# Kernel tuning notes

Hardware: AMD Instinct MI355X
Metric: run time of the kernel (lower is better)

## Reference

```python
import jax, jax.numpy as jnp
import numpy as np

VOCAB, EMBED, HIDDEN = 32000, 1024, 1024
BATCH, SEQ = 64, 128
PAD_IDX = 0


def setup_inputs() -> dict:
    key = jax.random.key(0)
    k_in, k_emb, k_wih, k_whh, k_bih, k_bhh = jax.random.split(key, 6)
    inputs = jax.random.randint(k_in, (BATCH, SEQ), 0, VOCAB)
    emb = jax.random.normal(k_emb, (VOCAB, EMBED), dtype=jnp.float32)
    emb = emb.at[PAD_IDX].set(0.0)  # nn.Embedding zeros the padding_idx row
    s = 1.0 / np.sqrt(HIDDEN).astype(np.float32)  # torch LSTMCell init bound
    W_ih = jax.random.uniform(k_wih, (4 * HIDDEN, EMBED), minval=-s, maxval=s, dtype=jnp.float32)
    W_hh = jax.random.uniform(k_whh, (4 * HIDDEN, HIDDEN), minval=-s, maxval=s, dtype=jnp.float32)
    b_ih = jax.random.uniform(k_bih, (4 * HIDDEN,), minval=-s, maxval=s, dtype=jnp.float32)
    b_hh = jax.random.uniform(k_bhh, (4 * HIDDEN,), minval=-s, maxval=s, dtype=jnp.float32)
    return {"emb": emb, "W_ih": W_ih, "W_hh": W_hh, "b_ih": b_ih, "b_hh": b_hh, "inputs": inputs}


def reference(emb, W_ih, W_hh, b_ih, b_hh, inputs):
    # Embedding lookup: [B, S, E] -> time-major [S, B, E]
    x = jnp.swapaxes(emb[inputs], 0, 1)
    B = inputs.shape[0]
    H = W_hh.shape[1]
    h0 = jnp.zeros((B, H), dtype=emb.dtype)
    c0 = jnp.zeros((B, H), dtype=emb.dtype)

    def step(carry, xt):
        h, c = carry
        # torch LSTMCell gate order: i, f, g, o
        gates = xt @ W_ih.T + b_ih + h @ W_hh.T + b_hh  # [B, 4H]
        i, f, g, o = jnp.split(gates, 4, axis=-1)
        i = jax.nn.sigmoid(i)
        f = jax.nn.sigmoid(f)
        g = jnp.tanh(g)
        o = jax.nn.sigmoid(o)
        c2 = f * c + i * g
        h2 = o * jnp.tanh(c2)
        # NOTE: original's h_c_mask is all-zeros (its fill loop only writes
        # zeros), so torch.where always selects the new state -> no masking.
        return (h2, c2), None

    (h, c), _ = jax.lax.scan(step, (h0, c0), x)
    return (h, c)
```

## Files before the change

### kernel.cpp

```cpp
#include <hip/hip_runtime.h>
#include <hip/hip_bf16.h>

#define EMB   1024
#define HID   1024
#define NBATCH 64
#define SEQ   128
#define NGATE 4096
#define NBLK  128

typedef __attribute__((ext_vector_type(8))) short bf16x8;
typedef __attribute__((ext_vector_type(4))) float f32x4;

__device__ __forceinline__ unsigned short f2bf(float f) {
    unsigned int u = __float_as_uint(f);
    unsigned int r = (u + 0x7FFFu + ((u >> 16) & 1u)) >> 16;
    return (unsigned short)r;
}

__device__ __forceinline__ bf16x8 pack8(float4 a, float4 b) {
    bf16x8 r;
    r[0] = (short)f2bf(a.x); r[1] = (short)f2bf(a.y);
    r[2] = (short)f2bf(a.z); r[3] = (short)f2bf(a.w);
    r[4] = (short)f2bf(b.x); r[5] = (short)f2bf(b.y);
    r[6] = (short)f2bf(b.z); r[7] = (short)f2bf(b.w);
    return r;
}

__device__ __forceinline__ float sigmoidf_(float x) { return 1.0f / (1.0f + __expf(-x)); }
__device__ __forceinline__ float tanhf_(float x)    { return 1.0f - 2.0f / (1.0f + __expf(2.0f * x)); }


__global__ void gather_x(const float* __restrict__ emb, const int* __restrict__ inp,
                         unsigned short* __restrict__ xbf) {
    int m = blockIdx.x;
    int t = m >> 6, b = m & 63;
    int tok = inp[b * SEQ + t];
    float4 v = ((const float4*)(emb + (long)tok * EMB))[threadIdx.x];
    ushort4 o;
    o.x = f2bf(v.x); o.y = f2bf(v.y); o.z = f2bf(v.z); o.w = f2bf(v.w);
    ((ushort4*)(xbf + (long)m * EMB))[threadIdx.x] = o;
}

__global__ void conv_w(const float* __restrict__ w, unsigned short* __restrict__ wbf) {
    long i = (long)blockIdx.x * 1024 + (long)threadIdx.x * 4;
    float4 v = *(const float4*)(w + i);
    ushort4 o;
    o.x = f2bf(v.x); o.y = f2bf(v.y); o.z = f2bf(v.z); o.w = f2bf(v.w);
    *(ushort4*)(wbf + i) = o;
}

__global__ void bsum_k(const float* __restrict__ bi, const float* __restrict__ bh,
                       float* __restrict__ bs) {
    int i = blockIdx.x * 256 + threadIdx.x;
    bs[i] = bi[i] + bh[i];
}

__global__ __launch_bounds__(256) void gemm_xw(const unsigned short* __restrict__ A,
                                               const unsigned short* __restrict__ Bw,
                                               const float* __restrict__ bsum,
                                               float* __restrict__ XW) {
    __shared__ unsigned short As[128][40];
    __shared__ unsigned short Bs[128][40];
    int bx = blockIdx.x;
    int by = blockIdx.y;
    int tid = threadIdx.x;
    int w = tid >> 6, l = tid & 63;
    int wm = w >> 1, wn = w & 1;
    int lr = l & 15, lk = l >> 4;

    f32x4 acc[4][4];
#pragma unroll
    for (int ni = 0; ni < 4; ++ni) {
        float bsv = bsum[bx * 128 + wn * 64 + ni * 16 + lr];
#pragma unroll
        for (int mi = 0; mi < 4; ++mi) {
            acc[mi][ni][0] = bsv; acc[mi][ni][1] = bsv;
            acc[mi][ni][2] = bsv; acc[mi][ni][3] = bsv;
        }
    }

    int sr = tid >> 1;
    int sc = (tid & 1) * 16;
    const unsigned short* ga = A  + (long)(by * 128 + sr) * 1024 + sc;
    const unsigned short* gb = Bw + (long)(bx * 128 + sr) * 1024 + sc;

    for (int kt = 0; kt < 32; ++kt) {
        uint4 va0 = *(const uint4*)(ga);
        uint4 va1 = *(const uint4*)(ga + 8);
        uint4 vb0 = *(const uint4*)(gb);
        uint4 vb1 = *(const uint4*)(gb + 8);
        *(uint4*)&As[sr][sc]     = va0;
        *(uint4*)&As[sr][sc + 8] = va1;
        *(uint4*)&Bs[sr][sc]     = vb0;
        *(uint4*)&Bs[sr][sc + 8] = vb1;
        __syncthreads();

        bf16x8 af[4], bfr[4];
#pragma unroll
        for (int mi = 0; mi < 4; ++mi)
            af[mi] = *(const bf16x8*)&As[wm * 64 + mi * 16 + lr][lk * 8];
#pragma unroll
        for (int ni = 0; ni < 4; ++ni)
            bfr[ni] = *(const bf16x8*)&Bs[wn * 64 + ni * 16 + lr][lk * 8];
#pragma unroll
        for (int mi = 0; mi < 4; ++mi)
#pragma unroll
            for (int ni = 0; ni < 4; ++ni)
                acc[mi][ni] = __builtin_amdgcn_mfma_f32_16x16x32_bf16(af[mi], bfr[ni], acc[mi][ni], 0, 0, 0);
        __syncthreads();
        ga += 32; gb += 32;
    }

#pragma unroll
    for (int mi = 0; mi < 4; ++mi) {
        int mg = by * 128 + wm * 64 + mi * 16 + lk * 4;
        int tt = mg >> 6;
        int bb = mg & 63;
#pragma unroll
        for (int ni = 0; ni < 4; ++ni) {
            int nn = bx * 128 + wn * 64 + ni * 16 + lr;
            *(f32x4*)(XW + (long)tt * (NGATE * 64) + (long)nn * 64 + bb) = acc[mi][ni];
        }
    }
}

__global__ __launch_bounds__(512) void lstm_rec(const float* __restrict__ Whh,
                                                const float* __restrict__ XW,
                                                unsigned short* __restrict__ hseq,
                                                unsigned* __restrict__ flags,
                                                float* __restrict__ out) {
    __shared__ float Glds[32][68];
    __shared__ unsigned short Hs[64][8];

    int tid = threadIdx.x;
    int w = tid >> 6, l = tid & 63;
    int lr = l & 15, lk = l >> 4;
    int bg = w & 3, ng = w >> 2;
    int g = blockIdx.x;
    unsigned* flags1 = flags;
    unsigned* flags2 = flags + 128;
    int grp = g >> 3;
    int rep = g & 15;
    bool leader = (g & 7) == 0;

    int nl = ng * 16 + lr;
    int q = nl >> 3, u = nl & 7;
    long nrow = (long)(q * 1024 + g * 8 + u) * 1024;
    bf16x8 wf[32];
#pragma unroll
    for (int kk = 0; kk < 32; ++kk) {
        int k0 = kk * 32 + lk * 8;
        float4 w0 = *(const float4*)(Whh + nrow + k0);
        float4 w1 = *(const float4*)(Whh + nrow + k0 + 4);
        wf[kk] = pack8(w0, w1);
    }

    float c = 0.0f;
    int brow = bg * 16 + lr;

    for (int t = 0; t < SEQ; ++t) {
        const uint4* hc = (const uint4*)hseq + (long)t * 8192;

        float px[4];
#pragma unroll
        for (int qq = 0; qq < 4; ++qq)
            px[qq] = XW[(long)t * (NGATE * 64) +
                        (long)(qq * 1024 + g * 8 + w) * 64 + l];

        f32x4 acc0 = {0.f, 0.f, 0.f, 0.f}, acc1 = {0.f, 0.f, 0.f, 0.f};
#pragma unroll
        for (int kk = 0; kk < 32; kk += 2) {
            union { uint4 u4; bf16x8 v; } ua, ub;
            ua.u4 = hc[(kk * 4 + lk) * 64 + brow];
            ub.u4 = hc[((kk + 1) * 4 + lk) * 64 + brow];
            acc0 = __builtin_amdgcn_mfma_f32_16x16x32_bf16(ua.v, wf[kk],     acc0, 0, 0, 0);
            acc1 = __builtin_amdgcn_mfma_f32_16x16x32_bf16(ub.v, wf[kk + 1], acc1, 0, 0, 0);
        }
        f32x4 gacc = acc0 + acc1;
        *(f32x4*)&Glds[ng * 16 + lr][bg * 16 + lk * 4] = gacc;
        __syncthreads();

        float p[4];
#pragma unroll
        for (int qq = 0; qq < 4; ++qq)
            p[qq] = Glds[qq * 8 + w][l] + px[qq];
        float ig = sigmoidf_(p[0]);
        float fg = sigmoidf_(p[1]);
        float gg = tanhf_(p[2]);
        float og = sigmoidf_(p[3]);
        c = fg * c + ig * gg;
        float h = og * tanhf_(c);

        if (t == SEQ - 1) {
            out[l * HID + g * 8 + w] = h;
            out[NBATCH * HID + l * HID + g * 8 + w] = c;
        } else {
            Hs[l][w] = f2bf(h);
            __syncthreads();
            unsigned tv = (unsigned)(t + 1);

            if (tid < 64) {
                unsigned long long* hn = (unsigned long long*)hseq +
                                         (long)(t + 1) * 16384 + (long)g * 128;
                const unsigned long long* hsu = (const unsigned long long*)Hs;
                __hip_atomic_store(&hn[tid * 2],     hsu[tid * 2],
                                   __ATOMIC_RELAXED, __HIP_MEMORY_SCOPE_AGENT);
                __hip_atomic_store(&hn[tid * 2 + 1], hsu[tid * 2 + 1],
                                   __ATOMIC_RELAXED, __HIP_MEMORY_SCOPE_AGENT);
                asm volatile("s_waitcnt vmcnt(0)" ::: "memory");
                if (tid == 0)
                    __hip_atomic_store(&flags1[g], tv,
                                       __ATOMIC_RELAXED, __HIP_MEMORY_SCOPE_AGENT);

                if (leader) {
                    if (tid < 2) {
                        const unsigned* fp = flags1 + g + tid * 4;
                        long spins = 0;
                        for (;;) {
                            uint4 fv;
                            asm volatile("global_load_dwordx4 %0, %1, off sc0 sc1\n\t"
                                         "s_waitcnt vmcnt(0)"
                                         : "=v"(fv) : "v"(fp) : "memory");
                            __builtin_amdgcn_sched_barrier(0);
                            unsigned mn  = fv.x < fv.y ? fv.x : fv.y;
                            unsigned mn2 = fv.z < fv.w ? fv.z : fv.w;
                            if (mn2 < mn) mn = mn2;
                            if (mn >= tv) break;
                            if (++spins > 500000L) break;
                            __builtin_amdgcn_s_sleep(1);
                        }
                    }
                    if (tid < 16)
                        __hip_atomic_store(&flags2[tid * 16 + grp], tv,
                                           __ATOMIC_RELAXED, __HIP_MEMORY_SCOPE_AGENT);
                }

                if (tid < 4) {
                    const unsigned* fp = flags2 + rep * 16 + tid * 4;
                    long spins = 0;
                    for (;;) {
                        uint4 fv;
                        asm volatile("global_load_dwordx4 %0, %1, off sc0 sc1\n\t"
                                     "s_waitcnt vmcnt(0)"
                                     : "=v"(fv) : "v"(fp) : "memory");
                        __builtin_amdgcn_sched_barrier(0);
                        unsigned mn  = fv.x < fv.y ? fv.x : fv.y;
                        unsigned mn2 = fv.z < fv.w ? fv.z : fv.w;
                        if (mn2 < mn) mn = mn2;
                        if (mn >= tv) break;
                        if (++spins > 500000L) break;
                        __builtin_amdgcn_s_sleep(1);
                    }
                }
            }
            __syncthreads();
        }
    }
}

extern "C" void kernel_launch(void* const* d_in, const int* in_sizes, int n_in,
                              void* d_out, int out_size, void* d_ws, size_t ws_size,
                              hipStream_t stream) {
    const float* emb  = (const float*)d_in[0];
    const float* W_ih = (const float*)d_in[1];
    const float* W_hh = (const float*)d_in[2];
    const float* b_ih = (const float*)d_in[3];
    const float* b_hh = (const float*)d_in[4];
    const int*   inp  = (const int*)d_in[5];
    float* out = (float*)d_out;

    char* ws = (char*)d_ws;
    float*          XW   = (float*)ws;
    unsigned short* Xbf  = (unsigned short*)(ws + 134217728);
    unsigned short* Wbf  = (unsigned short*)(ws + 150994944);
    float*          bs   = (float*)(ws + 159383552);
    unsigned short* hseq = (unsigned short*)(ws + 159399936);
    unsigned*       flags= (unsigned*)(ws + 176177152);

    hipMemsetAsync(flags, 0, 1536, stream);
    hipMemsetAsync(hseq, 0, NBATCH * HID * sizeof(unsigned short), stream);
    gather_x<<<SEQ * NBATCH, 256, 0, stream>>>(emb, inp, Xbf);
    conv_w<<<NGATE, 256, 0, stream>>>(W_ih, Wbf);
    bsum_k<<<16, 256, 0, stream>>>(b_ih, b_hh, bs);
    gemm_xw<<<dim3(32, 64), 256, 0, stream>>>(Xbf, Wbf, bs, XW);
    lstm_rec<<<NBLK, 512, 0, stream>>>(W_hh, XW, hseq, flags, out);
}
```

Before: 813.3 us.

## Fuse input projection into recurrent kernel and overlap it with grid barrier wait

Removes the separate input-projection GEMM and its large fp32 intermediate, and computes each block's x·W_ih contribution inside the recurrent kernel. The contribution for step t+1 is computed with MFMA while waiting on the cross-block barrier, so it hides in what was idle spin time. Bias is now added from registers. The cost is that W_ih rows and X are reread from global memory each step instead of being held in registers, which may lengthen the critical path if the barrier wait is short.

```diff
diff --git a/kernel.cpp b/kernel.cpp
--- a/kernel.cpp
+++ b/kernel.cpp
@@ -55,77 +55,25 @@
     bs[i] = bi[i] + bh[i];
 }
 
-__global__ __launch_bounds__(256) void gemm_xw(const unsigned short* __restrict__ A,
-                                               const unsigned short* __restrict__ Bw,
-                                               const float* __restrict__ bsum,
-                                               float* __restrict__ XW) {
-    __shared__ unsigned short As[128][40];
-    __shared__ unsigned short Bs[128][40];
-    int bx = blockIdx.x;
-    int by = blockIdx.y;
-    int tid = threadIdx.x;
-    int w = tid >> 6, l = tid & 63;
-    int wm = w >> 1, wn = w & 1;
-    int lr = l & 15, lk = l >> 4;
-
-    f32x4 acc[4][4];
-#pragma unroll
-    for (int ni = 0; ni < 4; ++ni) {
-        float bsv = bsum[bx * 128 + wn * 64 + ni * 16 + lr];
-#pragma unroll
-        for (int mi = 0; mi < 4; ++mi) {
-            acc[mi][ni][0] = bsv; acc[mi][ni][1] = bsv;
-            acc[mi][ni][2] = bsv; acc[mi][ni][3] = bsv;
-        }
+__device__ __forceinline__ void accum_x(const unsigned short* __restrict__ xr,
+                                        const unsigned short* __restrict__ wr,
+                                        int lk, f32x4& a0, f32x4& a1) {
+#pragma unroll
+    for (int kk = 0; kk < 32; kk += 2) {
+        union { uint4 u4; bf16x8 v; } xa, xb, wa, wb;
+        xa.u4 = *(const uint4*)(xr + kk * 32 + lk * 8);
+        xb.u4 = *(const uint4*)(xr + (kk + 1) * 32 + lk * 8);
+        wa.u4 = *(const uint4*)(wr + kk * 32 + lk * 8);
+        wb.u4 = *(const uint4*)(wr + (kk + 1) * 32 + lk * 8);
+        a0 = __builtin_amdgcn_mfma_f32_16x16x32_bf16(xa.v, wa.v, a0, 0, 0, 0);
+        a1 = __builtin_amdgcn_mfma_f32_16x16x32_bf16(xb.v, wb.v, a1, 0, 0, 0);
     }
-
-    int sr = tid >> 1;
-    int sc = (tid & 1) * 16;
-    const unsigned short* ga = A  + (long)(by * 128 + sr) * 1024 + sc;
-    const unsigned short* gb = Bw + (long)(bx * 128 + sr) * 1024 + sc;
-
-    for (int kt = 0; kt < 32; ++kt) {
-        uint4 va0 = *(const uint4*)(ga);
-        uint4 va1 = *(const uint4*)(ga + 8);
-        uint4 vb0 = *(const uint4*)(gb);
-        uint4 vb1 = *(const uint4*)(gb + 8);
-        *(uint4*)&As[sr][sc]     = va0;
-        *(uint4*)&As[sr][sc + 8] = va1;
-        *(uint4*)&Bs[sr][sc]     = vb0;
-        *(uint4*)&Bs[sr][sc + 8] = vb1;
-        __syncthreads();
-
-        bf16x8 af[4], bfr[4];
-#pragma unroll
-        for (int mi = 0; mi < 4; ++mi)
-            af[mi] = *(const bf16x8*)&As[wm * 64 + mi * 16 + lr][lk * 8];
-#pragma unroll
-        for (int ni = 0; ni < 4; ++ni)
-            bfr[ni] = *(const bf16x8*)&Bs[wn * 64 + ni * 16 + lr][lk * 8];
-#pragma unroll
-        for (int mi = 0; mi < 4; ++mi)
-#pragma unroll
-            for (int ni = 0; ni < 4; ++ni)
-                acc[mi][ni] = __builtin_amdgcn_mfma_f32_16x16x32_bf16(af[mi], bfr[ni], acc[mi][ni], 0, 0, 0);
-        __syncthreads();
-        ga += 32; gb += 32;
-    }
-
-#pragma unroll
-    for (int mi = 0; mi < 4; ++mi) {
-        int mg = by * 128 + wm * 64 + mi * 16 + lk * 4;
-        int tt = mg >> 6;
-        int bb = mg & 63;
-#pragma unroll
-        for (int ni = 0; ni < 4; ++ni) {
-            int nn = bx * 128 + wn * 64 + ni * 16 + lr;
-            *(f32x4*)(XW + (long)tt * (NGATE * 64) + (long)nn * 64 + bb) = acc[mi][ni];
-        }
-    }
 }
 
 __global__ __launch_bounds__(512) void lstm_rec(const float* __restrict__ Whh,
-                                                const float* __restrict__ XW,
+                                                const unsigned short* __restrict__ Xbf,
+                                                const unsigned short* __restrict__ Wih,
+                                                const float* __restrict__ bsum,
                                                 unsigned short* __restrict__ hseq,
                                                 unsigned* __restrict__ flags,
                                                 float* __restrict__ out) {
@@ -154,36 +102,39 @@
         float4 w1 = *(const float4*)(Whh + nrow + k0 + 4);
         wf[kk] = pack8(w0, w1);
     }
+    const unsigned short* wr = Wih + nrow;
+
+    float bsv[4];
+#pragma unroll
+    for (int qq = 0; qq < 4; ++qq)
+        bsv[qq] = bsum[qq * 1024 + g * 8 + w];
 
     float c = 0.0f;
     int brow = bg * 16 + lr;
 
+    f32x4 axc0 = {0.f, 0.f, 0.f, 0.f}, axc1 = {0.f, 0.f, 0.f, 0.f};
+    accum_x(Xbf + (long)brow * 1024, wr, lk, axc0, axc1);
+
     for (int t = 0; t < SEQ; ++t) {
         const uint4* hc = (const uint4*)hseq + (long)t * 8192;
 
-        float px[4];
-#pragma unroll
-        for (int qq = 0; qq < 4; ++qq)
-            px[qq] = XW[(long)t * (NGATE * 64) +
-                        (long)(qq * 1024 + g * 8 + w) * 64 + l];
-
-        f32x4 acc0 = {0.f, 0.f, 0.f, 0.f}, acc1 = {0.f, 0.f, 0.f, 0.f};
+        f32x4 ah0 = {0.f, 0.f, 0.f, 0.f}, ah1 = {0.f, 0.f, 0.f, 0.f};
 #pragma unroll
         for (int kk = 0; kk < 32; kk += 2) {
             union { uint4 u4; bf16x8 v; } ua, ub;
             ua.u4 = hc[(kk * 4 + lk) * 64 + brow];
             ub.u4 = hc[((kk + 1) * 4 + lk) * 64 + brow];
-            acc0 = __builtin_amdgcn_mfma_f32_16x16x32_bf16(ua.v, wf[kk],     acc0, 0, 0, 0);
-            acc1 = __builtin_amdgcn_mfma_f32_16x16x32_bf16(ub.v, wf[kk + 1], acc1, 0, 0, 0);
+            ah0 = __builtin_amdgcn_mfma_f32_16x16x32_bf16(ua.v, wf[kk],     ah0, 0, 0, 0);
+            ah1 = __builtin_amdgcn_mfma_f32_16x16x32_bf16(ub.v, wf[kk + 1], ah1, 0, 0, 0);
         }
-        f32x4 gacc = acc0 + acc1;
+        f32x4 gacc = (axc0 + axc1) + (ah0 + ah1);
         *(f32x4*)&Glds[ng * 16 + lr][bg * 16 + lk * 4] = gacc;
         __syncthreads();
 
         float p[4];
 #pragma unroll
         for (int qq = 0; qq < 4; ++qq)
-            p[qq] = Glds[qq * 8 + w][l] + px[qq];
+            p[qq] = Glds[qq * 8 + w][l] + bsv[qq];
         float ig = sigmoidf_(p[0]);
         float fg = sigmoidf_(p[1]);
         float gg = tanhf_(p[2]);
@@ -211,7 +162,6 @@
                 if (tid == 0)
                     __hip_atomic_store(&flags1[g], tv,
                                        __ATOMIC_RELAXED, __HIP_MEMORY_SCOPE_AGENT);
-
                 if (leader) {
                     if (tid < 2) {
                         const unsigned* fp = flags1 + g + tid * 4;
@@ -234,26 +184,30 @@
                         __hip_atomic_store(&flags2[tid * 16 + grp], tv,
                                            __ATOMIC_RELAXED, __HIP_MEMORY_SCOPE_AGENT);
                 }
-
-                if (tid < 4) {
-                    const unsigned* fp = flags2 + rep * 16 + tid * 4;
-                    long spins = 0;
-                    for (;;) {
-                        uint4 fv;
-                        asm volatile("global_load_dwordx4 %0, %1, off sc0 sc1\n\t"
-                                     "s_waitcnt vmcnt(0)"
-                                     : "=v"(fv) : "v"(fp) : "memory");
-                        __builtin_amdgcn_sched_barrier(0);
-                        unsigned mn  = fv.x < fv.y ? fv.x : fv.y;
-                        unsigned mn2 = fv.z < fv.w ? fv.z : fv.w;
-                        if (mn2 < mn) mn = mn2;
-                        if (mn >= tv) break;
-                        if (++spins > 500000L) break;
-                        __builtin_amdgcn_s_sleep(1);
-                    }
+            }
+
+            f32x4 axn0 = {0.f, 0.f, 0.f, 0.f}, axn1 = {0.f, 0.f, 0.f, 0.f};
+            accum_x(Xbf + ((long)(t + 1) * 64 + brow) * 1024, wr, lk, axn0, axn1);
+
+            if (tid < 4) {
+                const unsigned* fp = flags2 + rep * 16 + tid * 4;
+                long spins = 0;
+                for (;;) {
+                    uint4 fv;
+                    asm volatile("global_load_dwordx4 %0, %1, off sc0 sc1\n\t"
+                                 "s_waitcnt vmcnt(0)"
+                                 : "=v"(fv) : "v"(fp) : "memory");
+                    __builtin_amdgcn_sched_barrier(0);
+                    unsigned mn  = fv.x < fv.y ? fv.x : fv.y;
+                    unsigned mn2 = fv.z < fv.w ? fv.z : fv.w;
+                    if (mn2 < mn) mn = mn2;
+                    if (mn >= tv) break;
+                    if (++spins > 500000L) break;
+                    __builtin_amdgcn_s_sleep(1);
                 }
             }
             __syncthreads();
+            axc0 = axn0; axc1 = axn1;
         }
     }
 }
@@ -270,18 +224,16 @@
     float* out = (float*)d_out;
 
     char* ws = (char*)d_ws;
-    float*          XW   = (float*)ws;
-    unsigned short* Xbf  = (unsigned short*)(ws + 134217728);
-    unsigned short* Wbf  = (unsigned short*)(ws + 150994944);
-    float*          bs   = (float*)(ws + 159383552);
-    unsigned short* hseq = (unsigned short*)(ws + 159399936);
-    unsigned*       flags= (unsigned*)(ws + 176177152);
+    unsigned short* Xbf  = (unsigned short*)ws;
+    unsigned short* Wbf  = (unsigned short*)(ws + 16777216);
+    float*          bs   = (float*)(ws + 25165824);
+    unsigned short* hseq = (unsigned short*)(ws + 25182208);
+    unsigned*       flags= (unsigned*)(ws + 41959424);
 
     hipMemsetAsync(flags, 0, 1536, stream);
     hipMemsetAsync(hseq, 0, NBATCH * HID * sizeof(unsigned short), stream);
     gather_x<<<SEQ * NBATCH, 256, 0, stream>>>(emb, inp, Xbf);
     conv_w<<<NGATE, 256, 0, stream>>>(W_ih, Wbf);
     bsum_k<<<16, 256, 0, stream>>>(b_ih, b_hh, bs);
-    gemm_xw<<<dim3(32, 64), 256, 0, stream>>>(Xbf, Wbf, bs, XW);
-    lstm_rec<<<NBLK, 512, 0, stream>>>(W_hh, XW, hseq, flags, out);
-}
+    lstm_rec<<<NBLK, 512, 0, stream>>>(W_hh, Xbf, Wbf, bs, hseq, flags, out);
+}
```

New measurement: 2.359 ms. +190.0%, slower.
